# Optimization experiments

Hardware: AMD Instinct MI355X
Metric: run time of the kernel (lower is better)

Reference implementation:

```python
import jax, jax.numpy as jnp
import numpy as np

BANDWIDTH = 1.0
EPS = 1e-20


def setup_inputs() -> dict:
    key = jax.random.key(0)
    k1, k2, k3 = jax.random.split(key, 3)
    test_X = jax.random.normal(k1, (8192, 64), dtype=jnp.float32)
    train_X = jax.random.normal(k2, (16384, 64), dtype=jnp.float32)
    sample_weight = jax.random.uniform(k3, (16384,), dtype=jnp.float32)
    return {"test_X": test_X, "train_X": train_X, "sample_weight": sample_weight}


def reference(test_X, train_X, sample_weight):
    # test_X: [m, d], train_X: [n, d], sample_weight: [n]
    d = train_X.shape[1]
    h = jnp.float32(BANDWIDTH)
    # weights are normalized; with weights, n is treated as 1 => log(n) = 0
    w = sample_weight / jnp.sum(sample_weight)
    Z = 0.5 * d * jnp.log(2.0 * jnp.float32(np.pi)) + d * jnp.log(h)
    # squared L2 distances via expansion (avoids [m, n, d] intermediate)
    t2 = jnp.sum(test_X * test_X, axis=-1)  # [m]
    r2 = jnp.sum(train_X * train_X, axis=-1)  # [n]
    cross = test_X @ train_X.T  # [m, n]
    sq = (t2[:, None] + r2[None, :] - 2.0 * cross) / (h * h)  # [m, n]
    val = -0.5 * sq - Z  # [m, n]
    # weighted, numerically-stable log-sum-exp over train dim
    m_max = jnp.max(val, axis=-1, keepdims=True)  # [m, 1]
    s = jnp.sum(jnp.exp(val - m_max) * w[None, :], axis=-1)  # [m]
    return m_max[:, 0] + jnp.log(s + EPS)
```

## Files before the change

kernel.cpp:

```cpp
#include <hip/hip_runtime.h>
#include <hip/hip_bf16.h>
#include <math.h>

#define M 8192
#define N 16384
#define D 64
#define ZC 58.81206612509905f
#define B0 24.0f
#define LOG2E 1.4426950408889634f
#define HL2E 0.7213475204444817f
#define LN2 0.6931471805599453f

#define PCH 32
#define NCHK (N / PCH)

typedef short v8bf __attribute__((ext_vector_type(8)));
typedef float v16f __attribute__((ext_vector_type(16)));

#define B_AU2  0
#define B_LW2  32768
#define B_PART 98304
#define B_TB   1146880
#define B_TR   2195456

__global__ __launch_bounds__(256) void gk_prep(const float* __restrict__ testX,
                                               const float* __restrict__ trainX,
                                               const float* __restrict__ sw,
                                               __hip_bfloat16* __restrict__ tb,
                                               __hip_bfloat16* __restrict__ rb,
                                               float* __restrict__ au2,
                                               float* __restrict__ lw2) {
    const int tid = threadIdx.x;
    const int e = tid & 7;
    if (blockIdx.x < M / 32) {
        const int row = blockIdx.x * 32 + (tid >> 3);
        const float4* p = reinterpret_cast<const float4*>(testX + (size_t)row * D + e * 8);
        float4 v0 = p[0], v1 = p[1];
        float t2 = v0.x * v0.x + v0.y * v0.y + v0.z * v0.z + v0.w * v0.w
                 + v1.x * v1.x + v1.y * v1.y + v1.z * v1.z + v1.w * v1.w;
        t2 += __shfl_xor(t2, 1, 64);
        t2 += __shfl_xor(t2, 2, 64);
        t2 += __shfl_xor(t2, 4, 64);
        if (e == 0) au2[row] = -HL2E * t2;
        union { __hip_bfloat16 h[8]; uint4 u; } cv;
        cv.h[0] = __float2bfloat16(v0.x * LOG2E);
        cv.h[1] = __float2bfloat16(v0.y * LOG2E);
        cv.h[2] = __float2bfloat16(v0.z * LOG2E);
        cv.h[3] = __float2bfloat16(v0.w * LOG2E);
        cv.h[4] = __float2bfloat16(v1.x * LOG2E);
        cv.h[5] = __float2bfloat16(v1.y * LOG2E);
        cv.h[6] = __float2bfloat16(v1.z * LOG2E);
        cv.h[7] = __float2bfloat16(v1.w * LOG2E);
        *reinterpret_cast<uint4*>(tb + (size_t)row * D + e * 8) = cv.u;
    } else {
        const int row = (blockIdx.x - M / 32) * 32 + (tid >> 3);
        const float4* p = reinterpret_cast<const float4*>(trainX + (size_t)row * D + e * 8);
        float4 v0 = p[0], v1 = p[1];
        float r2 = v0.x * v0.x + v0.y * v0.y + v0.z * v0.z + v0.w * v0.w
                 + v1.x * v1.x + v1.y * v1.y + v1.z * v1.z + v1.w * v1.w;
        r2 += __shfl_xor(r2, 1, 64);
        r2 += __shfl_xor(r2, 2, 64);
        r2 += __shfl_xor(r2, 4, 64);
        if (e == 0) lw2[row] = __builtin_amdgcn_logf(sw[row]) - HL2E * r2 + B0;
        union { __hip_bfloat16 h[8]; uint4 u; } cv;
        cv.h[0] = __float2bfloat16(v0.x);
        cv.h[1] = __float2bfloat16(v0.y);
        cv.h[2] = __float2bfloat16(v0.z);
        cv.h[3] = __float2bfloat16(v0.w);
        cv.h[4] = __float2bfloat16(v1.x);
        cv.h[5] = __float2bfloat16(v1.y);
        cv.h[6] = __float2bfloat16(v1.z);
        cv.h[7] = __float2bfloat16(v1.w);
        *reinterpret_cast<uint4*>(rb + (size_t)row * D + e * 8) = cv.u;
    }
}

__device__ __forceinline__ void dma16(const void* g, void* l) {
    __builtin_amdgcn_global_load_lds(
        (const __attribute__((address_space(1))) unsigned int*)g,
        (__attribute__((address_space(3))) unsigned int*)l, 16, 0, 0);
}

__device__ __forceinline__ void dma_tile(const __hip_bfloat16* tr, int nt,
                                         char* Bsb, int w, int lane) {
#pragma unroll
    for (int i = 0; i < 4; ++i) {
        const int g = w * 4 + i;
        const __hip_bfloat16* gp =
            tr + (size_t)(nt + g * 8 + (lane & 7)) * D + (lane >> 3) * 8;
        dma16(gp, Bsb + g * 1024);
    }
}

__device__ __forceinline__ void compute_tile(const char* Bs,
                                             const float* __restrict__ lwp,
                                             const v8bf af[4], float srun[16],
                                             int c, int h) {
#pragma unroll
    for (int s = 0; s < 4; ++s) {
        const float lwv = lwp[s * 32 + c];
        v16f acc;
#pragma unroll
        for (int r = 0; r < 16; ++r) acc[r] = lwv;
#pragma unroll
        for (int t = 0; t < 4; ++t) {
            const v8bf bf = *reinterpret_cast<const v8bf*>(
                Bs + (s * 4 + (c >> 3)) * 1024 + (2 * t + h) * 128 + (c & 7) * 16);
            acc = __builtin_amdgcn_mfma_f32_32x32x16_bf16(af[t], bf, acc, 0, 0, 0);
        }
#pragma unroll
        for (int r = 0; r < 16; ++r)
            srun[r] += __builtin_amdgcn_exp2f(acc[r]);
    }
}

__global__ __launch_bounds__(256, 4) void gk_main(const __hip_bfloat16* __restrict__ ta,
                                                  const __hip_bfloat16* __restrict__ tr,
                                                  const float* __restrict__ lw2,
                                                  float* __restrict__ part) {
    __shared__ __align__(16) char smem[32768];
    const int tid = threadIdx.x;
    const int w = tid >> 6;
    const int lane = tid & 63;
    const int c = lane & 31;
    const int h = lane >> 5;

    const int bid = blockIdx.x;
    const int xcd = bid & 7;
    const int j = bid >> 3;
    const int chunk = xcd * 4 + (j & 3);
    const int m0 = (j >> 2) * 128;
    const int n0 = chunk * NCHK;

    char* const Bs0 = smem;
    char* const Bs1 = smem + 16384;

    dma_tile(tr, n0, Bs0, w, lane);

    const __hip_bfloat16* arow = ta + (size_t)(m0 + w * 32 + c) * D;
    v8bf af[4];
#pragma unroll
    for (int t = 0; t < 4; ++t)
        af[t] = *reinterpret_cast<const v8bf*>(arow + (2 * t + h) * 8);

    float srun[16];
#pragma unroll
    for (int r = 0; r < 16; ++r) srun[r] = 0.f;

    __syncthreads();
    dma_tile(tr, n0 + 128, Bs1, w, lane);
    compute_tile(Bs0, lw2 + n0, af, srun, c, h);
    __syncthreads();
    dma_tile(tr, n0 + 256, Bs0, w, lane);
    compute_tile(Bs1, lw2 + n0 + 128, af, srun, c, h);
    __syncthreads();
    dma_tile(tr, n0 + 384, Bs1, w, lane);
    compute_tile(Bs0, lw2 + n0 + 256, af, srun, c, h);
    __syncthreads();
    compute_tile(Bs1, lw2 + n0 + 384, af, srun, c, h);

    __syncthreads();
    float* red = reinterpret_cast<float*>(smem);
#pragma unroll
    for (int r = 0; r < 16; ++r) {
        int rowl = (r & 3) + 8 * (r >> 2) + 4 * h;
        red[(w * 32 + rowl) * 33 + c] = srun[r];
    }
    __syncthreads();
    if (tid < 128) {
        float G = 0.f;
#pragma unroll
        for (int c2 = 0; c2 < 32; ++c2) G += red[tid * 33 + c2];
        part[(size_t)chunk * M + m0 + tid] = G;
    }
}

__global__ __launch_bounds__(256) void gk_merge(const float* __restrict__ part,
                                                const float* __restrict__ au2,
                                                const float* __restrict__ sw,
                                                float* __restrict__ out) {
    __shared__ float red[256];
    const int tid = threadIdx.x;
    float s = 0.f;
    const float4* p4 = reinterpret_cast<const float4*>(sw);
    for (int i = tid; i < N / 4; i += 256) {
        float4 v = p4[i];
        s += v.x + v.y + v.z + v.w;
    }
    red[tid] = s;
    __syncthreads();
    for (int off = 128; off > 0; off >>= 1) {
        if (tid < off) red[tid] += red[tid + off];
        __syncthreads();
    }
    const float W = red[0];

    const int r = blockIdx.x * 256 + tid;
    float G = 0.f;
#pragma unroll
    for (int p = 0; p < PCH; ++p) G += part[(size_t)p * M + r];
    out[r] = LN2 * (au2[r] + __builtin_amdgcn_logf(fmaxf(G, 1e-30f)) - B0
                   - __builtin_amdgcn_logf(W)) - ZC;
}

extern "C" void kernel_launch(void* const* d_in, const int* in_sizes, int n_in,
                              void* d_out, int out_size, void* d_ws, size_t ws_size,
                              hipStream_t stream) {
    const float* testX  = (const float*)d_in[0];
    const float* trainX = (const float*)d_in[1];
    const float* sw     = (const float*)d_in[2];
    float* out = (float*)d_out;
    char* wsb = (char*)d_ws;

    float* au2  = (float*)(wsb + B_AU2);
    float* lw2  = (float*)(wsb + B_LW2);
    float* part = (float*)(wsb + B_PART);
    __hip_bfloat16* tb = (__hip_bfloat16*)(wsb + B_TB);
    __hip_bfloat16* rb = (__hip_bfloat16*)(wsb + B_TR);

    gk_prep<<<M / 32 + N / 32, 256, 0, stream>>>(testX, trainX, sw, tb, rb, au2, lw2);
    gk_main<<<(M / 128) * PCH, 256, 0, stream>>>(tb, rb, lw2, part);
    gk_merge<<<M / 256, 256, 0, stream>>>(part, au2, sw, out);
}
```

Baseline: 100.5 us.

## Double rows per block and fuse merge into main kernel via atomic counter

Each block now covers 256 test rows instead of 128, with each wave computing two 32-row MFMA tiles that share the loaded train fragments. This halves LDS traffic for B per output and halves the block count. The separate merge kernel is removed. The last block to finish a row slice, found with an atomic counter that is zeroed in the prep kernel, does the final reduction and log. This saves a kernel launch but adds register pressure, which may hurt occupancy under launch_bounds(256,4), and puts serial tail work on the last block of each slice.

```diff
diff --git a/kernel.cpp b/kernel.cpp
--- a/kernel.cpp
+++ b/kernel.cpp
@@ -13,15 +13,18 @@
 
 #define PCH 32
 #define NCHK (N / PCH)
+#define RB 256
+#define MSL (M / RB)
 
 typedef short v8bf __attribute__((ext_vector_type(8)));
 typedef float v16f __attribute__((ext_vector_type(16)));
 
 #define B_AU2  0
 #define B_LW2  32768
-#define B_PART 98304
-#define B_TB   1146880
-#define B_TR   2195456
+#define B_CNT  98304
+#define B_PART 131072
+#define B_TB   1179648
+#define B_TR   2228224
 
 __global__ __launch_bounds__(256) void gk_prep(const float* __restrict__ testX,
                                                const float* __restrict__ trainX,
@@ -29,9 +32,11 @@
                                                __hip_bfloat16* __restrict__ tb,
                                                __hip_bfloat16* __restrict__ rb,
                                                float* __restrict__ au2,
-                                               float* __restrict__ lw2) {
+                                               float* __restrict__ lw2,
+                                               unsigned int* __restrict__ cnt) {
     const int tid = threadIdx.x;
     const int e = tid & 7;
+    if (blockIdx.x == 0 && tid < MSL) cnt[tid] = 0;
     if (blockIdx.x < M / 32) {
         const int row = blockIdx.x * 32 + (tid >> 3);
         const float4* p = reinterpret_cast<const float4*>(testX + (size_t)row * D + e * 8);
@@ -94,31 +99,43 @@
 
 __device__ __forceinline__ void compute_tile(const char* Bs,
                                              const float* __restrict__ lwp,
-                                             const v8bf af[4], float srun[16],
+                                             const v8bf af[2][4], float srun[2][16],
                                              int c, int h) {
 #pragma unroll
     for (int s = 0; s < 4; ++s) {
         const float lwv = lwp[s * 32 + c];
-        v16f acc;
-#pragma unroll
-        for (int r = 0; r < 16; ++r) acc[r] = lwv;
-#pragma unroll
-        for (int t = 0; t < 4; ++t) {
-            const v8bf bf = *reinterpret_cast<const v8bf*>(
+        v8bf bf[4];
+#pragma unroll
+        for (int t = 0; t < 4; ++t)
+            bf[t] = *reinterpret_cast<const v8bf*>(
                 Bs + (s * 4 + (c >> 3)) * 1024 + (2 * t + h) * 128 + (c & 7) * 16);
-            acc = __builtin_amdgcn_mfma_f32_32x32x16_bf16(af[t], bf, acc, 0, 0, 0);
+        v16f a0, a1;
+#pragma unroll
+        for (int r = 0; r < 16; ++r) { a0[r] = lwv; a1[r] = lwv; }
+#pragma unroll
+        for (int t = 0; t < 4; ++t)
+            a0 = __builtin_amdgcn_mfma_f32_32x32x16_bf16(af[0][t], bf[t], a0, 0, 0, 0);
+#pragma unroll
+        for (int t = 0; t < 4; ++t)
+            a1 = __builtin_amdgcn_mfma_f32_32x32x16_bf16(af[1][t], bf[t], a1, 0, 0, 0);
+#pragma unroll
+        for (int r = 0; r < 16; ++r) {
+            srun[0][r] += __builtin_amdgcn_exp2f(a0[r]);
+            srun[1][r] += __builtin_amdgcn_exp2f(a1[r]);
         }
-#pragma unroll
-        for (int r = 0; r < 16; ++r)
-            srun[r] += __builtin_amdgcn_exp2f(acc[r]);
     }
 }
 
 __global__ __launch_bounds__(256, 4) void gk_main(const __hip_bfloat16* __restrict__ ta,
                                                   const __hip_bfloat16* __restrict__ tr,
                                                   const float* __restrict__ lw2,
-                                                  float* __restrict__ part) {
-    __shared__ __align__(16) char smem[32768];
+                                                  const float* __restrict__ au2,
+                                                  const float* __restrict__ sw,
+                                                  float* __restrict__ part,
+                                                  unsigned int* __restrict__ cnt,
+                                                  float* __restrict__ out) {
+    __shared__ __align__(16) char smem[33792];
+    __shared__ int sflag;
     const int tid = threadIdx.x;
     const int w = tid >> 6;
     const int lane = tid & 63;
@@ -129,7 +146,8 @@
     const int xcd = bid & 7;
     const int j = bid >> 3;
     const int chunk = xcd * 4 + (j & 3);
-    const int m0 = (j >> 2) * 128;
+    const int msl = j >> 2;
+    const int m0 = msl * RB;
     const int n0 = chunk * NCHK;
 
     char* const Bs0 = smem;
@@ -137,15 +155,19 @@
 
     dma_tile(tr, n0, Bs0, w, lane);
 
-    const __hip_bfloat16* arow = ta + (size_t)(m0 + w * 32 + c) * D;
-    v8bf af[4];
-#pragma unroll
-    for (int t = 0; t < 4; ++t)
-        af[t] = *reinterpret_cast<const v8bf*>(arow + (2 * t + h) * 8);
-
-    float srun[16];
-#pragma unroll
-    for (int r = 0; r < 16; ++r) srun[r] = 0.f;
+    v8bf af[2][4];
+    const __hip_bfloat16* ar0 = ta + (size_t)(m0 + w * 64 + c) * D;
+#pragma unroll
+    for (int t = 0; t < 4; ++t) {
+        af[0][t] = *reinterpret_cast<const v8bf*>(ar0 + (2 * t + h) * 8);
+        af[1][t] = *reinterpret_cast<const v8bf*>(ar0 + 32 * D + (2 * t + h) * 8);
+    }
+
+    float srun[2][16];
+#pragma unroll
+    for (int ms = 0; ms < 2; ++ms)
+#pragma unroll
+        for (int r = 0; r < 16; ++r) srun[ms][r] = 0.f;
 
     __syncthreads();
     dma_tile(tr, n0 + 128, Bs1, w, lane);
@@ -162,45 +184,50 @@
     __syncthreads();
     float* red = reinterpret_cast<float*>(smem);
 #pragma unroll
-    for (int r = 0; r < 16; ++r) {
-        int rowl = (r & 3) + 8 * (r >> 2) + 4 * h;
-        red[(w * 32 + rowl) * 33 + c] = srun[r];
-    }
-    __syncthreads();
-    if (tid < 128) {
-        float G = 0.f;
-#pragma unroll
-        for (int c2 = 0; c2 < 32; ++c2) G += red[tid * 33 + c2];
-        part[(size_t)chunk * M + m0 + tid] = G;
-    }
-}
-
-__global__ __launch_bounds__(256) void gk_merge(const float* __restrict__ part,
-                                                const float* __restrict__ au2,
-                                                const float* __restrict__ sw,
-                                                float* __restrict__ out) {
-    __shared__ float red[256];
-    const int tid = threadIdx.x;
+    for (int ms = 0; ms < 2; ++ms)
+#pragma unroll
+        for (int r = 0; r < 16; ++r) {
+            int row = w * 64 + ms * 32 + (r & 3) + 8 * (r >> 2) + 4 * h;
+            red[row * 33 + c] = srun[ms][r];
+        }
+    __syncthreads();
+    float G = 0.f;
+#pragma unroll
+    for (int c2 = 0; c2 < 32; ++c2) G += red[tid * 33 + c2];
+    part[(size_t)chunk * M + m0 + tid] = G;
+
+    __syncthreads();
+    if (tid == 0) {
+        __threadfence();
+        unsigned int prev = atomicAdd(&cnt[msl], 1u);
+        sflag = (prev == PCH - 1);
+    }
+    __syncthreads();
+    if (!sflag) return;
+    __threadfence();
+
     float s = 0.f;
     const float4* p4 = reinterpret_cast<const float4*>(sw);
-    for (int i = tid; i < N / 4; i += 256) {
-        float4 v = p4[i];
+#pragma unroll
+    for (int i = 0; i < 16; ++i) {
+        float4 v = p4[tid + 256 * i];
         s += v.x + v.y + v.z + v.w;
     }
-    red[tid] = s;
+    float* wr = reinterpret_cast<float*>(smem);
+    wr[tid] = s;
     __syncthreads();
     for (int off = 128; off > 0; off >>= 1) {
-        if (tid < off) red[tid] += red[tid + off];
+        if (tid < off) wr[tid] += wr[tid + off];
         __syncthreads();
     }
-    const float W = red[0];
-
-    const int r = blockIdx.x * 256 + tid;
-    float G = 0.f;
-#pragma unroll
-    for (int p = 0; p < PCH; ++p) G += part[(size_t)p * M + r];
-    out[r] = LN2 * (au2[r] + __builtin_amdgcn_logf(fmaxf(G, 1e-30f)) - B0
-                   - __builtin_amdgcn_logf(W)) - ZC;
+    const float W = wr[0];
+
+    volatile const float* pv = part;
+    float Gt = 0.f;
+#pragma unroll
+    for (int p = 0; p < PCH; ++p) Gt += pv[(size_t)p * M + m0 + tid];
+    out[m0 + tid] = LN2 * (au2[m0 + tid] + __builtin_amdgcn_logf(fmaxf(Gt, 1e-30f))
+                           - B0 - __builtin_amdgcn_logf(W)) - ZC;
 }
 
 extern "C" void kernel_launch(void* const* d_in, const int* in_sizes, int n_in,
@@ -214,11 +241,11 @@
 
     float* au2  = (float*)(wsb + B_AU2);
     float* lw2  = (float*)(wsb + B_LW2);
+    unsigned int* cnt = (unsigned int*)(wsb + B_CNT);
     float* part = (float*)(wsb + B_PART);
     __hip_bfloat16* tb = (__hip_bfloat16*)(wsb + B_TB);
     __hip_bfloat16* rb = (__hip_bfloat16*)(wsb + B_TR);
 
-    gk_prep<<<M / 32 + N / 32, 256, 0, stream>>>(testX, trainX, sw, tb, rb, au2, lw2);
-    gk_main<<<(M / 128) * PCH, 256, 0, stream>>>(tb, rb, lw2, part);
-    gk_merge<<<M / 256, 256, 0, stream>>>(part, au2, sw, out);
-}
+    gk_prep<<<M / 32 + N / 32, 256, 0, stream>>>(testX, trainX, sw, tb, rb, au2, lw2, cnt);
+    gk_main<<<MSL * PCH, 256, 0, stream>>>(tb, rb, lw2, au2, sw, part, cnt, out);
+}
```

Result: slower. 138.4 us (+37.7%).
